# Optimization experiments

Measured on AMD Instinct MI355X. Metric: run time of the kernel, lower is better.

## Reference

```python
import jax, jax.numpy as jnp
import numpy as np

HIDDEN = 256
MAX_POS = 2000  # table has MAX_POS + 1 rows


def get_sinusoid_encoding_table(n_position, d_hid):
    pos = np.arange(n_position, dtype=np.float64)[:, None]
    i = np.arange(d_hid)[None, :]
    angle = pos / np.power(10000.0, 2.0 * (i // 2) / d_hid)
    table = np.zeros((n_position, d_hid), dtype=np.float32)
    table[:, 0::2] = np.sin(angle[:, 0::2])
    table[:, 1::2] = np.cos(angle[:, 1::2])
    return jnp.asarray(table)


def setup_inputs() -> dict:
    key = jax.random.key(0)
    k1, k2 = jax.random.split(key)
    B, T = 64, 160
    x = jax.random.normal(k1, (B, T, HIDDEN), dtype=jnp.float32)
    duration = jax.random.randint(k2, (B, T), 0, 12, dtype=jnp.int64 if jax.config.jax_enable_x64 else jnp.int32)
    position_enc = get_sinusoid_encoding_table(MAX_POS + 1, HIDDEN)
    return {"x": x, "position_enc": position_enc, "duration": duration, "max_len": 2000}


def reference(x, position_enc, duration, max_len):
    # x: [B, T, H], duration: [B, T] ints, max_len: python int
    B, T, H = x.shape
    csum = jnp.cumsum(duration, axis=1)            # inclusive cumsum [B, T]
    excl = csum - duration                          # exclusive cumsum [B, T]
    mel_len = csum[:, -1]                           # [B]
    frames = jnp.arange(max_len)                    # [L]
    # token index owning each output frame: smallest t with csum[t] > frame
    idx = jax.vmap(lambda c: jnp.searchsorted(c, frames, side='right'))(csum)  # [B, L]
    idx = jnp.minimum(idx, T - 1)
    valid = frames[None, :] < mel_len[:, None]      # [B, L]
    # gather expanded features
    out = jnp.take_along_axis(x, idx[..., None], axis=1)          # [B, L, H]
    # per-token local position -> sinusoid table row
    pos_within = frames[None, :] - jnp.take_along_axis(excl, idx, axis=1)  # [B, L]
    pos_within = jnp.where(valid, pos_within, 0)
    pos = position_enc[pos_within]                                 # [B, L, H]
    out = jnp.where(valid[..., None], out, 0.0)
    pos = jnp.where(valid[..., None], pos, 0.0)
    return out, pos, mel_len
```

## Files before the change

### kernel.cpp

```cpp
#include <hip/hip_runtime.h>

constexpr int B      = 64;
constexpr int T      = 160;
constexpr int H      = 256;
constexpr int MAXLEN = 2000;
constexpr int FPB    = 16;
constexpr int NTH    = 256;

__global__ __launch_bounds__(NTH) void lr_kernel(
    const float* __restrict__ x,
    const float* __restrict__ pos_enc,
    const int*   __restrict__ duration,
    float*       __restrict__ out)
{
    __shared__ int s_scan[NTH];
    __shared__ int s_csum[T];
    __shared__ int s_excl[T];

    const int b   = blockIdx.y;
    const int tid = threadIdx.x;

    int d = (tid < T) ? duration[b * T + tid] : 0;
    s_scan[tid] = d;
    __syncthreads();
    #pragma unroll
    for (int off = 1; off < NTH; off <<= 1) {
        int v   = s_scan[tid];
        int add = (tid >= off) ? s_scan[tid - off] : 0;
        __syncthreads();
        s_scan[tid] = v + add;
        __syncthreads();
    }
    if (tid < T) {
        s_csum[tid] = s_scan[tid];
        s_excl[tid] = s_scan[tid] - d;
    }
    __syncthreads();

    const int mel_len = s_csum[T - 1];

    if (blockIdx.x == 0 && tid == 0) {
        out[(size_t)2 * B * MAXLEN * H + b] = (float)mel_len;
    }

    const int wave = tid >> 6;
    const int lane = tid & 63;

    const size_t out_base = (size_t)b * MAXLEN * H;
    const size_t pos_base = (size_t)B * MAXLEN * H + out_base;
    const int f0 = blockIdx.x * FPB;

    for (int i = wave; i < FPB; i += 4) {
        const int f = f0 + i;
        if (f >= MAXLEN) break;
        const bool valid = (f < mel_len);

        int lo = 0, hi = T;
        while (lo < hi) {
            int mid = (lo + hi) >> 1;
            if (s_csum[mid] <= f) lo = mid + 1; else hi = mid;
        }
        const int idx = min(lo, T - 1);

        float4 xo = make_float4(0.f, 0.f, 0.f, 0.f);
        float4 po = xo;
        if (valid) {
            const int pw = f - s_excl[idx];
            xo = ((const float4*)(x + ((size_t)b * T + idx) * H))[lane];
            po = ((const float4*)(pos_enc + (size_t)pw * H))[lane];
        }
        ((float4*)(out + out_base + (size_t)f * H))[lane] = xo;
        ((float4*)(out + pos_base + (size_t)f * H))[lane] = po;
    }
}

extern "C" void kernel_launch(void* const* d_in, const int* in_sizes, int n_in,
                              void* d_out, int out_size, void* d_ws, size_t ws_size,
                              hipStream_t stream)
{
    const float* x        = (const float*)d_in[0];
    const float* pos_enc  = (const float*)d_in[1];
    const int*   duration = (const int*)d_in[2];
    float*       out      = (float*)d_out;

    dim3 grid((MAXLEN + FPB - 1) / FPB, B);
    lr_kernel<<<grid, NTH, 0, stream>>>(x, pos_enc, duration, out);
}
```

Before: 267.7 us.

## Precompute per-frame token map in a separate kernel, simplify expand kernel

```diff
diff --git a/kernel.cpp b/kernel.cpp
--- a/kernel.cpp
+++ b/kernel.cpp
@@ -6,6 +6,80 @@
 constexpr int MAXLEN = 2000;
 constexpr int FPB    = 16;
 constexpr int NTH    = 256;
+
+typedef float floatx4 __attribute__((ext_vector_type(4)));
+
+__global__ __launch_bounds__(NTH) void build_map_kernel(
+    const int* __restrict__ duration,
+    int*       __restrict__ map,
+    float*     __restrict__ out)
+{
+    __shared__ int s_scan[NTH];
+    const int b   = blockIdx.x;
+    const int tid = threadIdx.x;
+
+    int d = (tid < T) ? duration[b * T + tid] : 0;
+    s_scan[tid] = d;
+    __syncthreads();
+    #pragma unroll
+    for (int off = 1; off < NTH; off <<= 1) {
+        int v   = s_scan[tid];
+        int add = (tid >= off) ? s_scan[tid - off] : 0;
+        __syncthreads();
+        s_scan[tid] = v + add;
+        __syncthreads();
+    }
+    const int csum    = s_scan[tid];
+    const int excl    = csum - d;
+    const int mel_len = s_scan[T - 1];
+
+    if (tid == 0)
+        out[(size_t)2 * B * MAXLEN * H + b] = (float)mel_len;
+
+    int* bm = map + b * MAXLEN;
+
+    for (int f = mel_len + tid; f < MAXLEN; f += NTH)
+        bm[f] = -1;
+
+    if (tid < T) {
+        for (int f = excl; f < csum; ++f)
+            bm[f] = (tid << 8) | (f - excl);
+    }
+}
+
+__global__ __launch_bounds__(NTH) void expand_kernel(
+    const float* __restrict__ x,
+    const float* __restrict__ pos_enc,
+    const int*   __restrict__ map,
+    float*       __restrict__ out)
+{
+    const int tid  = threadIdx.x;
+    const int b    = blockIdx.y;
+    const int wave = tid >> 6;
+    const int lane = tid & 63;
+
+    const size_t out_base = (size_t)b * MAXLEN * H;
+    const size_t pos_base = (size_t)B * MAXLEN * H + out_base;
+    const int f0 = blockIdx.x * FPB;
+    const int* bm = map + b * MAXLEN;
+
+    #pragma unroll
+    for (int i = 0; i < FPB / 4; ++i) {
+        const int f = f0 + wave + 4 * i;
+        const int m = bm[f];
+
+        floatx4 xo = (floatx4)0.f;
+        floatx4 po = (floatx4)0.f;
+        if (m >= 0) {
+            const int t  = m >> 8;
+            const int pw = m & 255;
+            xo = ((const floatx4*)(x       + ((size_t)b * T + t) * H))[lane];
+            po = ((const floatx4*)(pos_enc + (size_t)pw      * H))[lane];
+        }
+        __builtin_nontemporal_store(xo, (floatx4*)(out + out_base + (size_t)f * H) + lane);
+        __builtin_nontemporal_store(po, (floatx4*)(out + pos_base + (size_t)f * H) + lane);
+    }
+}
 
 __global__ __launch_bounds__(NTH) void lr_kernel(
     const float* __restrict__ x,
@@ -38,14 +112,12 @@
     __syncthreads();
 
     const int mel_len = s_csum[T - 1];
-
     if (blockIdx.x == 0 && tid == 0) {
         out[(size_t)2 * B * MAXLEN * H + b] = (float)mel_len;
     }
 
     const int wave = tid >> 6;
     const int lane = tid & 63;
-
     const size_t out_base = (size_t)b * MAXLEN * H;
     const size_t pos_base = (size_t)B * MAXLEN * H + out_base;
     const int f0 = blockIdx.x * FPB;
@@ -83,6 +155,13 @@
     const int*   duration = (const int*)d_in[2];
     float*       out      = (float*)d_out;
 
-    dim3 grid((MAXLEN + FPB - 1) / FPB, B);
-    lr_kernel<<<grid, NTH, 0, stream>>>(x, pos_enc, duration, out);
+    const size_t map_bytes = (size_t)B * MAXLEN * sizeof(int);
+    if (d_ws != nullptr && ws_size >= map_bytes) {
+        int* map = (int*)d_ws;
+        build_map_kernel<<<dim3(B), NTH, 0, stream>>>(duration, map, out);
+        expand_kernel<<<dim3(MAXLEN / FPB, B), NTH, 0, stream>>>(x, pos_enc, map, out);
+    } else {
+        dim3 grid((MAXLEN + FPB - 1) / FPB, B);
+        lr_kernel<<<grid, NTH, 0, stream>>>(x, pos_enc, duration, out);
+    }
 }
```

Measured after the change: 279.6 us. 1.04x slower.

## Persistent grid with per-wave batched gathers to amortize per-block scan

Applied to the files above, without the earlier changes.

```diff
diff --git a/kernel.cpp b/kernel.cpp
--- a/kernel.cpp
+++ b/kernel.cpp
@@ -6,8 +6,9 @@
 constexpr int MAXLEN = 2000;
 constexpr int FPB    = 16;
 constexpr int NTH    = 256;
+constexpr int TPB_X  = 32;
 
-__global__ __launch_bounds__(NTH) void lr_kernel(
+__global__ __launch_bounds__(NTH) void lr_fused_kernel(
     const float* __restrict__ x,
     const float* __restrict__ pos_enc,
     const int*   __restrict__ duration,
@@ -38,39 +39,53 @@
     __syncthreads();
 
     const int mel_len = s_csum[T - 1];
-
-    if (blockIdx.x == 0 && tid == 0) {
+    if (blockIdx.x == 0 && tid == 0)
         out[(size_t)2 * B * MAXLEN * H + b] = (float)mel_len;
-    }
 
     const int wave = tid >> 6;
     const int lane = tid & 63;
 
-    const size_t out_base = (size_t)b * MAXLEN * H;
-    const size_t pos_base = (size_t)B * MAXLEN * H + out_base;
-    const int f0 = blockIdx.x * FPB;
+    const float* xb   = x   + (size_t)b * T * H;
+    float*       outb = out + (size_t)b * MAXLEN * H;
+    float*       posb = outb + (size_t)B * MAXLEN * H;
 
-    for (int i = wave; i < FPB; i += 4) {
-        const int f = f0 + i;
-        if (f >= MAXLEN) break;
-        const bool valid = (f < mel_len);
+    constexpr int NTILE = MAXLEN / FPB;
+    for (int tx = blockIdx.x; tx < NTILE; tx += TPB_X) {
+        const int fw = tx * FPB + 4 * wave;
 
-        int lo = 0, hi = T;
-        while (lo < hi) {
-            int mid = (lo + hi) >> 1;
-            if (s_csum[mid] <= f) lo = mid + 1; else hi = mid;
+        int   tk[4], pw[4];
+        float sc[4];
+        #pragma unroll
+        for (int j = 0; j < 4; ++j) {
+            const int f = fw + j;
+            int lo = 0, hi = T;
+            while (lo < hi) {
+                int mid = (lo + hi) >> 1;
+                if (s_csum[mid] <= f) lo = mid + 1; else hi = mid;
+            }
+            const int idx = min(lo, T - 1);
+            const bool valid = (f < mel_len);
+            tk[j] = valid ? idx : 0;
+            pw[j] = valid ? (f - s_excl[idx]) : 0;
+            sc[j] = valid ? 1.0f : 0.0f;
         }
-        const int idx = min(lo, T - 1);
 
-        float4 xo = make_float4(0.f, 0.f, 0.f, 0.f);
-        float4 po = xo;
-        if (valid) {
-            const int pw = f - s_excl[idx];
-            xo = ((const float4*)(x + ((size_t)b * T + idx) * H))[lane];
-            po = ((const float4*)(pos_enc + (size_t)pw * H))[lane];
+        float4 xo[4], po[4];
+        #pragma unroll
+        for (int j = 0; j < 4; ++j) {
+            xo[j] = ((const float4*)(xb      + (size_t)tk[j] * H))[lane];
+            po[j] = ((const float4*)(pos_enc + (size_t)pw[j] * H))[lane];
         }
-        ((float4*)(out + out_base + (size_t)f * H))[lane] = xo;
-        ((float4*)(out + pos_base + (size_t)f * H))[lane] = po;
+        #pragma unroll
+        for (int j = 0; j < 4; ++j) {
+            const int f = fw + j;
+            float4 a = make_float4(xo[j].x * sc[j], xo[j].y * sc[j],
+                                   xo[j].z * sc[j], xo[j].w * sc[j]);
+            float4 p = make_float4(po[j].x * sc[j], po[j].y * sc[j],
+                                   po[j].z * sc[j], po[j].w * sc[j]);
+            ((float4*)(outb + (size_t)f * H))[lane] = a;
+            ((float4*)(posb + (size_t)f * H))[lane] = p;
+        }
     }
 }
 
@@ -83,6 +98,5 @@
     const int*   duration = (const int*)d_in[2];
     float*       out      = (float*)d_out;
 
-    dim3 grid((MAXLEN + FPB - 1) / FPB, B);
-    lr_kernel<<<grid, NTH, 0, stream>>>(x, pos_enc, duration, out);
+    lr_fused_kernel<<<dim3(TPB_X, B), NTH, 0, stream>>>(x, pos_enc, duration, out);
 }
```

Result: slower. 274.1 us (+2.4%).
